# Performance work log

Measured on AMD Instinct MI355X. Metric: run time of the kernel, lower is better.

Reference implementation:

```python
import jax, jax.numpy as jnp
import numpy as np

BN_EPS = 1e-5
L2_EPS = 1e-12


def setup_inputs() -> dict:
    key = jax.random.key(0)
    ks = jax.random.split(key, 4)
    B, C, H, W = 16, 384, 56, 56
    x = jax.random.normal(ks[0], (B, C, H, W), dtype=jnp.float32)
    w_qkv = jax.random.normal(ks[1], (3 * C, C), dtype=jnp.float32) * (1.0 / np.sqrt(C))
    b_qkv = jnp.zeros((3 * C,), dtype=jnp.float32)
    w_proj = jax.random.normal(ks[2], (C, C), dtype=jnp.float32) * (1.0 / np.sqrt(C))
    b_proj = jnp.zeros((C,), dtype=jnp.float32)
    bn_gamma = jnp.ones((C,), dtype=jnp.float32)
    bn_beta = jnp.zeros((C,), dtype=jnp.float32)
    bn_mean = jnp.zeros((C,), dtype=jnp.float32)
    bn_var = jnp.ones((C,), dtype=jnp.float32)
    temperature = jnp.ones((1,), dtype=jnp.float32)
    return {"x": x, "w_qkv": w_qkv, "b_qkv": b_qkv, "w_proj": w_proj,
            "b_proj": b_proj, "bn_gamma": bn_gamma, "bn_beta": bn_beta,
            "bn_mean": bn_mean, "bn_var": bn_var, "temperature": temperature}


def _l2norm_lastdim(t):
    # F.normalize(t, dim=-1): divide by max(||t||_2, eps)
    n = jnp.sqrt(jnp.sum(t * t, axis=-1, keepdims=True))
    return t / jnp.maximum(n, L2_EPS)


def reference(x, w_qkv, b_qkv, w_proj, b_proj, bn_gamma, bn_beta, bn_mean, bn_var, temperature):
    B, C, H, W = x.shape
    N = H * W
    # BatchNorm2d (eval mode, running stats)
    scale = bn_gamma / jnp.sqrt(bn_var + BN_EPS)          # [C]
    shift = bn_beta - bn_mean * scale                     # [C]
    xn = x * scale[None, :, None, None] + shift[None, :, None, None]
    # 1x1 conv qkv: C -> 3C, operate on flattened spatial [B, C, N]
    xn_f = xn.reshape(B, C, N)
    qkv = jnp.einsum('oc,bcn->bon', w_qkv, xn_f) + b_qkv[None, :, None]  # [B,3C,N]
    q, k, v = qkv[:, :C], qkv[:, C:2 * C], qkv[:, 2 * C:]
    q = _l2norm_lastdim(q)                                # [B,C,N]
    k = _l2norm_lastdim(k)
    # channel-transposed attention: [B,C,C]
    logits = jnp.einsum('bcn,bdn->bcd', q, k) * temperature[0]
    attn = jax.nn.softmax(logits, axis=-1)
    fused = jnp.einsum('bcd,bdn->bcn', attn, v)           # [B,C,N]
    # 1x1 proj conv + residual
    out = jnp.einsum('oc,bcn->bon', w_proj, fused) + b_proj[None, :, None]
    return x + out.reshape(B, C, H, W)
```

## Files before the change

kernel.cpp:

```cpp
#include <hip/hip_runtime.h>

#define BATCH 16
#define CCH   384
#define NSP   3136
#define OQKV  1152

typedef unsigned short u16;
typedef float  f32x4  __attribute__((ext_vector_type(4)));
typedef __bf16 bf16x8 __attribute__((ext_vector_type(8)));

__device__ __forceinline__ float bf2f(u16 u) {
  union { unsigned int i; float f; } v; v.i = ((unsigned int)u) << 16; return v.f;
}
__device__ __forceinline__ u16 f2bf(float f) {
  union { float f; unsigned int i; } v; v.f = f;
  unsigned int i = v.i;
  return (u16)((i + 0x7fffu + ((i >> 16) & 1u)) >> 16);
}
__device__ __forceinline__ float rdf(const void* p, long i, bool bf) {
  return bf ? bf2f(((const u16*)p)[i]) : ((const float*)p)[i];
}

__global__ void transpose_kernel(const void* __restrict__ x, u16* __restrict__ xt,
                                 const u16* __restrict__ probe) {
  const bool bf = (probe[0] == 0x3F80u);
  __shared__ float Ls[32 * 65];
  const int t = threadIdx.x;
  const int n0 = blockIdx.x * 64, c0 = blockIdx.y * 32, b = blockIdx.z;
  {
    const int c_l = t >> 3, n8 = (t & 7) * 8;
    const long src = ((long)b * CCH + c0 + c_l) * NSP + n0 + n8;
    float v[8];
    if (bf) {
      union { uint4 q; u16 e[8]; } u; u.q = *(const uint4*)((const u16*)x + src);
      #pragma unroll
      for (int i = 0; i < 8; i++) v[i] = bf2f(u.e[i]);
    } else {
      float4 a = *(const float4*)((const float*)x + src);
      float4 c = *(const float4*)((const float*)x + src + 4);
      v[0]=a.x; v[1]=a.y; v[2]=a.z; v[3]=a.w; v[4]=c.x; v[5]=c.y; v[6]=c.z; v[7]=c.w;
    }
    #pragma unroll
    for (int i = 0; i < 8; i++) Ls[c_l * 65 + n8 + i] = v[i];
  }
  __syncthreads();
  {
    const int n_l = t >> 2, c8 = (t & 3) * 8;
    union { uint4 q; u16 e[8]; } o;
    #pragma unroll
    for (int i = 0; i < 8; i++) o.e[i] = f2bf(Ls[(c8 + i) * 65 + n_l]);
    *(uint4*)(xt + ((long)b * NSP + n0 + n_l) * CCH + c0 + c8) = o.q;
  }
}

__global__ void prep_kernel(const void* __restrict__ w_qkv, const void* __restrict__ b_qkv,
                            const void* __restrict__ gamma, const void* __restrict__ beta,
                            const void* __restrict__ mean,  const void* __restrict__ var,
                            const void* __restrict__ b_proj, const void* __restrict__ w_proj,
                            u16* __restrict__ w_eff, float* __restrict__ b_eff,
                            float* __restrict__ bproj_f, u16* __restrict__ wp_bf,
                            const u16* __restrict__ probe) {
  const bool bf = (probe[0] == 0x3F80u);
  __shared__ float s_scale[CCH], s_shift[CCH];
  const int tid = threadIdx.x;
  for (int c = tid; c < CCH; c += 128) {
    float g = rdf(gamma, c, bf), bt = rdf(beta, c, bf);
    float mn = rdf(mean, c, bf), vr = rdf(var, c, bf);
    float sc = g * rsqrtf(vr + 1e-5f);
    s_scale[c] = sc; s_shift[c] = bt - mn * sc;
  }
  __syncthreads();
  const int o = blockIdx.x;
  float part = 0.f;
  for (int c = tid; c < CCH; c += 128) {
    float w = rdf(w_qkv, (long)o * CCH + c, bf);
    w_eff[o * CCH + c] = f2bf(w * s_scale[c]);
    part += w * s_shift[c];
  }
  for (int off = 32; off > 0; off >>= 1) part += __shfl_down(part, off, 64);
  __shared__ float s_part[2];
  if ((tid & 63) == 0) s_part[tid >> 6] = part;
  __syncthreads();
  if (tid == 0) b_eff[o] = rdf(b_qkv, o, bf) + s_part[0] + s_part[1];
  if (o < CCH) {
    for (int c = tid; c < CCH; c += 128)
      wp_bf[o * CCH + c] = f2bf(rdf(w_proj, (long)o * CCH + c, bf));
  }
  if (o == 0) {
    for (int c = tid; c < CCH; c += 128) bproj_f[c] = rdf(b_proj, c, bf);
  }
}

template<int BM, int BN, int WGM, int WGN, int OUTM, bool BIASM, bool BIASN, bool RES>
__launch_bounds__(256)
__global__ void gemm_nt(const u16* __restrict__ A, const u16* __restrict__ B,
                        void* __restrict__ Cv,
                        const float* __restrict__ biasm, const float* __restrict__ biasn,
                        const void* __restrict__ resv,
                        int K, int lda, int ldb, int ldc,
                        long sA, long sB, long sC, long sRes, int zb,
                        const u16* __restrict__ probe) {
  constexpr int WM = BM / WGM, WN = BN / WGN;
  constexpr int FM = WM / 16,  FN = WN / 16;
  constexpr int NA = BM / 32,  NB = BN / 32;
  const bool f32io = (probe[0] != 0x3F80u);
  __shared__ u16 As[BM * 64];
  __shared__ u16 Bs[BN * 64];
  const int tid = threadIdx.x, wave = tid >> 6, lane = tid & 63;
  const int quad = lane >> 4, l16 = lane & 15;
  const int wm = wave / WGN, wn = wave % WGN;
  const int z = blockIdx.z;
  A += z * sA; B += z * sB;
  const long cOff = (long)(zb + z) * sC;
  const long rOff = (long)(zb + z) * sRes;
  const int m0 = blockIdx.x * BM, n0 = blockIdx.y * BN;

  f32x4 acc[FM][FN] = {};

  for (int k0 = 0; k0 < K; k0 += 64) {
    uint4 av[NA], bv[NB];
    #pragma unroll
    for (int p = 0; p < NA; p++) {
      int u = tid + p * 256;
      av[p] = *(const uint4*)(A + (long)(m0 + (u >> 3)) * lda + k0 + (u & 7) * 8);
    }
    #pragma unroll
    for (int p = 0; p < NB; p++) {
      int u = tid + p * 256;
      bv[p] = *(const uint4*)(B + (long)(n0 + (u >> 3)) * ldb + k0 + (u & 7) * 8);
    }
    #pragma unroll
    for (int p = 0; p < NA; p++) {
      int u = tid + p * 256, r = u >> 3;
      *(uint4*)&As[r * 64 + (((u & 7) ^ (r & 7)) << 3)] = av[p];
    }
    #pragma unroll
    for (int p = 0; p < NB; p++) {
      int u = tid + p * 256, r = u >> 3;
      *(uint4*)&Bs[r * 64 + (((u & 7) ^ (r & 7)) << 3)] = bv[p];
    }
    __syncthreads();

    #pragma unroll
    for (int t = 0; t < 2; t++) {
      bf16x8 af[FM], bfr[FN];
      #pragma unroll
      for (int f = 0; f < FM; f++) {
        int r = wm * WM + f * 16 + l16;
        af[f] = *(const bf16x8*)&As[r * 64 + (((t * 4 + quad) ^ (l16 & 7)) << 3)];
      }
      #pragma unroll
      for (int g = 0; g < FN; g++) {
        int r = wn * WN + g * 16 + l16;
        bfr[g] = *(const bf16x8*)&Bs[r * 64 + (((t * 4 + quad) ^ (l16 & 7)) << 3)];
      }
      #pragma unroll
      for (int f = 0; f < FM; f++)
        #pragma unroll
        for (int g = 0; g < FN; g++)
          acc[f][g] = __builtin_amdgcn_mfma_f32_16x16x32_bf16(af[f], bfr[g], acc[f][g], 0, 0, 0);
    }
    __syncthreads();
  }

  #pragma unroll
  for (int f = 0; f < FM; f++) {
    #pragma unroll
    for (int g = 0; g < FN; g++) {
      #pragma unroll
      for (int reg = 0; reg < 4; reg++) {
        int mm = m0 + wm * WM + f * 16 + quad * 4 + reg;
        int nn = n0 + wn * WN + g * 16 + l16;
        float v = acc[f][g][reg];
        if (BIASM) v += biasm[mm];
        if (BIASN) v += biasn[nn];
        long off = (long)mm * ldc + nn;
        if (RES) {
          long ro = rOff + off;
          v += f32io ? ((const float*)resv)[ro] : bf2f(((const u16*)resv)[ro]);
        }
        if (OUTM == 1)      ((float*)Cv)[cOff + off] = v;
        else if (OUTM == 2) { if (f32io) ((float*)Cv)[cOff + off] = v;
                              else       ((u16*)Cv)[cOff + off]   = f2bf(v); }
        else                ((u16*)Cv)[cOff + off] = f2bf(v);
      }
    }
  }
}

__global__ void norms_kernel(const u16* __restrict__ qk, float* __restrict__ invn) {
  const int row = blockIdx.x, b = blockIdx.y;
  const u16* p = qk + (long)b * 768 * NSP + (long)row * NSP;
  float s = 0.f;
  for (int i = threadIdx.x * 8; i < NSP; i += 256 * 8) {
    union { uint4 v; u16 u[8]; } x; x.v = *(const uint4*)(p + i);
    #pragma unroll
    for (int j = 0; j < 8; j++) { float t = bf2f(x.u[j]); s += t * t; }
  }
  for (int off = 32; off > 0; off >>= 1) s += __shfl_down(s, off, 64);
  __shared__ float sp[4];
  if ((threadIdx.x & 63) == 0) sp[threadIdx.x >> 6] = s;
  __syncthreads();
  if (threadIdx.x == 0) {
    float t = sp[0] + sp[1] + sp[2] + sp[3];
    invn[b * 768 + row] = 1.f / fmaxf(sqrtf(t), 1e-12f);
  }
}

__global__ void softmax_kernel(const float* __restrict__ logits, const float* __restrict__ invn,
                               const void* __restrict__ temp, u16* __restrict__ attn,
                               const u16* __restrict__ probe) {
  const bool bfm = (probe[0] == 0x3F80u);
  const int c = blockIdx.x, b = blockIdx.y;
  const float* row = logits + ((long)b * CCH + c) * CCH;
  const float rq = invn[b * 768 + c];
  const float T = rdf(temp, 0, bfm);
  const int tid = threadIdx.x;
  float v[3]; float mx = -1e30f;
  #pragma unroll
  for (int j = 0; j < 3; j++) {
    int d = tid + j * 128;
    float xv = row[d] * rq * invn[b * 768 + 384 + d] * T;
    v[j] = xv; mx = fmaxf(mx, xv);
  }
  for (int off = 32; off > 0; off >>= 1) mx = fmaxf(mx, __shfl_down(mx, off, 64));
  __shared__ float sm[2];
  if ((tid & 63) == 0) sm[tid >> 6] = mx;
  __syncthreads();
  mx = fmaxf(sm[0], sm[1]);
  float s = 0.f;
  #pragma unroll
  for (int j = 0; j < 3; j++) { v[j] = __expf(v[j] - mx); s += v[j]; }
  for (int off = 32; off > 0; off >>= 1) s += __shfl_down(s, off, 64);
  __shared__ float ss[2];
  if ((tid & 63) == 0) ss[tid >> 6] = s;
  __syncthreads();
  s = ss[0] + ss[1];
  const float inv = 1.f / s;
  u16* arow = attn + ((long)b * CCH + c) * CCH;
  #pragma unroll
  for (int j = 0; j < 3; j++) arow[tid + j * 128] = f2bf(v[j] * inv);
}

extern "C" void kernel_launch(void* const* d_in, const int* in_sizes, int n_in,
                              void* d_out, int out_size, void* d_ws, size_t ws_size,
                              hipStream_t stream) {
  const void* x      = d_in[0];
  const void* w_qkv  = d_in[1];
  const void* b_qkv  = d_in[2];
  const void* w_proj = d_in[3];
  const void* b_proj = d_in[4];
  const void* gamma  = d_in[5];
  const void* beta   = d_in[6];
  const void* mean   = d_in[7];
  const void* var    = d_in[8];
  const void* temp   = d_in[9];
  const u16* probe = (const u16*)gamma;

  const size_t SZ_XT    = (size_t)BATCH * NSP * CCH * 2;
  const size_t SZ_WEFF  = (size_t)OQKV * CCH * 2;
  const size_t SZ_WPBF  = (size_t)CCH * CCH * 2;
  const size_t SZ_BEFF  = (size_t)OQKV * 4;
  const size_t SZ_BPROJ = (size_t)CCH * 4;
  const size_t SZ_INVN  = (size_t)BATCH * 768 * 4;
  const size_t SZ_QK_B  = (size_t)768 * NSP * 2;
  const size_t SZ_VT_B  = (size_t)NSP * CCH * 2;
  const size_t SZ_FT_B  = (size_t)NSP * CCH * 2;
  const size_t SZ_LOG_B = (size_t)CCH * CCH * 4;
  const size_t SZ_ATT_B = (size_t)CCH * CCH * 2;
  const size_t P = SZ_QK_B + SZ_VT_B + SZ_FT_B + SZ_LOG_B + SZ_ATT_B;
  const size_t FIXED = SZ_XT + SZ_WEFF + SZ_WPBF + SZ_BEFF + SZ_BPROJ + SZ_INVN;

  long chunk = 1;
  if (ws_size >= FIXED + P) {
    chunk = (long)((ws_size - FIXED) / P);
    if (chunk > BATCH) chunk = BATCH;
    if (chunk < 1) chunk = 1;
  }

  char* ws = (char*)d_ws;
  u16*   xt      = (u16*)ws;   ws += SZ_XT;
  u16*   w_eff   = (u16*)ws;   ws += SZ_WEFF;
  u16*   wp_bf   = (u16*)ws;   ws += SZ_WPBF;
  float* b_eff   = (float*)ws; ws += SZ_BEFF;
  float* bproj_f = (float*)ws; ws += SZ_BPROJ;
  float* invn    = (float*)ws; ws += SZ_INVN;
  float* logits  = (float*)ws; ws += SZ_LOG_B * chunk;
  u16*   attn    = (u16*)ws;   ws += SZ_ATT_B * chunk;
  u16*   qk      = (u16*)ws;   ws += SZ_QK_B * chunk;
  u16*   v_t     = (u16*)ws;   ws += SZ_VT_B * chunk;
  u16*   fused_t = (u16*)ws;   ws += SZ_FT_B * chunk;

  transpose_kernel<<<dim3(NSP / 64, CCH / 32, BATCH), dim3(256), 0, stream>>>(x, xt, probe);
  prep_kernel<<<dim3(OQKV), dim3(128), 0, stream>>>(
      w_qkv, b_qkv, gamma, beta, mean, var, b_proj, w_proj,
      w_eff, b_eff, bproj_f, wp_bf, probe);

  const long sX  = (long)CCH * NSP;
  const long sXT = (long)NSP * CCH;
  const long sQK = (long)768 * NSP;
  const long sVT = (long)NSP * CCH;
  const long sFT = (long)NSP * CCH;
  const long sLG = (long)CCH * CCH;
  const long sAT = (long)CCH * CCH;

  for (long b0 = 0; b0 < BATCH; b0 += chunk) {
    const int nb = (int)((BATCH - b0) < chunk ? (BATCH - b0) : chunk);
    const u16* xtb = xt + b0 * sXT;

    gemm_nt<256, 64, 4, 1, 0, true, false, false>
        <<<dim3(3, 49, nb), dim3(256), 0, stream>>>(
        w_eff, xtb, qk, b_eff, nullptr, nullptr,
        CCH, CCH, CCH, NSP, 0L, sXT, sQK, 0L, 0, probe);

    gemm_nt<64, 384, 1, 4, 0, false, true, false>
        <<<dim3(49, 1, nb), dim3(256), 0, stream>>>(
        xtb, w_eff + (long)768 * CCH, v_t, nullptr, b_eff + 768, nullptr,
        CCH, CCH, CCH, CCH, sXT, 0L, sVT, 0L, 0, probe);

    norms_kernel<<<dim3(768, nb), dim3(256), 0, stream>>>(qk, invn + b0 * 768);

    gemm_nt<96, 96, 2, 2, 1, false, false, false>
        <<<dim3(4, 4, nb), dim3(256), 0, stream>>>(
        qk, qk + (long)CCH * NSP, logits, nullptr, nullptr, nullptr,
        NSP, NSP, NSP, CCH, sQK, sQK, sLG, 0L, 0, probe);

    softmax_kernel<<<dim3(CCH, nb), dim3(128), 0, stream>>>(
        logits, invn + b0 * 768, temp, attn, probe);

    gemm_nt<64, 384, 1, 4, 0, false, false, false>
        <<<dim3(49, 1, nb), dim3(256), 0, stream>>>(
        v_t, attn, fused_t, nullptr, nullptr, nullptr,
        CCH, CCH, CCH, CCH, sVT, sAT, sFT, 0L, 0, probe);

    gemm_nt<384, 64, 4, 1, 2, true, false, true>
        <<<dim3(1, 49, nb), dim3(256), 0, stream>>>(
        wp_bf, fused_t, d_out, bproj_f, nullptr, x,
        CCH, CCH, CCH, NSP, 0L, sFT, sX, sX, (int)b0, probe);
  }
}
```

Baseline: 456.8 us.

## Use direct global-to-LDS loads, split-K logits GEMM, and smaller GEMM tiles

The GEMM tile loads now use global_load_lds, which writes global memory straight into shared memory and skips the register staging. The XOR swizzle moves onto the global source address so the LDS layout stays the same. The long-K logits GEMM is split 7 ways with atomicAdd into a pre-zeroed fp32 buffer, giving the small 4x4 grid more blocks. Several 384-wide tiles are halved to 192 to raise block count and lower LDS use. In exchange the change adds an extra zeroing kernel and atomic contention, and the async LDS load is still followed by a plain __syncthreads with no explicit wait on the load counter.

```diff
diff --git a/kernel.cpp b/kernel.cpp
--- a/kernel.cpp
+++ b/kernel.cpp
@@ -19,6 +19,12 @@
 }
 __device__ __forceinline__ float rdf(const void* p, long i, bool bf) {
   return bf ? bf2f(((const u16*)p)[i]) : ((const float*)p)[i];
+}
+
+__device__ __forceinline__ void gload_lds16(const u16* g, u16* l) {
+  __builtin_amdgcn_global_load_lds(
+      (const __attribute__((address_space(1))) void*)g,
+      (__attribute__((address_space(3))) void*)l, 16, 0, 0);
 }
 
 __global__ void transpose_kernel(const void* __restrict__ x, u16* __restrict__ xt,
@@ -91,7 +97,13 @@
   }
 }
 
-template<int BM, int BN, int WGM, int WGN, int OUTM, bool BIASM, bool BIASN, bool RES>
+__global__ void zero_kernel(float4* __restrict__ p, long n4) {
+  for (long i = (long)blockIdx.x * blockDim.x + threadIdx.x; i < n4;
+       i += (long)gridDim.x * blockDim.x)
+    p[i] = make_float4(0.f, 0.f, 0.f, 0.f);
+}
+
+template<int BM, int BN, int WGM, int WGN, int OUTM, bool BIASM, bool BIASN, bool RES, int KS>
 __launch_bounds__(256)
 __global__ void gemm_nt(const u16* __restrict__ A, const u16* __restrict__ B,
                         void* __restrict__ Cv,
@@ -104,41 +116,41 @@
   constexpr int FM = WM / 16,  FN = WN / 16;
   constexpr int NA = BM / 32,  NB = BN / 32;
   const bool f32io = (probe[0] != 0x3F80u);
-  __shared__ u16 As[BM * 64];
-  __shared__ u16 Bs[BN * 64];
+  __shared__ __align__(16) u16 As[BM * 64];
+  __shared__ __align__(16) u16 Bs[BN * 64];
   const int tid = threadIdx.x, wave = tid >> 6, lane = tid & 63;
   const int quad = lane >> 4, l16 = lane & 15;
   const int wm = wave / WGN, wn = wave % WGN;
-  const int z = blockIdx.z;
+  int z = blockIdx.z, kc = 0;
+  if (KS > 1) { kc = z % KS; z /= KS; }
   A += z * sA; B += z * sB;
   const long cOff = (long)(zb + z) * sC;
   const long rOff = (long)(zb + z) * sRes;
   const int m0 = blockIdx.x * BM, n0 = blockIdx.y * BN;
+  const int kLen = K / KS, kBeg = kc * kLen;
+
+  const u16* ag[NA]; u16* al[NA];
+  const u16* bg[NB]; u16* bl[NB];
+  #pragma unroll
+  for (int p = 0; p < NA; p++) {
+    int u = tid + p * 256, r = u >> 3, k8 = u & 7;
+    ag[p] = A + (long)(m0 + r) * lda + kBeg + ((k8 ^ (r & 7)) << 3);
+    al[p] = &As[(wave * 64 + p * 256) * 8];
+  }
+  #pragma unroll
+  for (int p = 0; p < NB; p++) {
+    int u = tid + p * 256, r = u >> 3, k8 = u & 7;
+    bg[p] = B + (long)(n0 + r) * ldb + kBeg + ((k8 ^ (r & 7)) << 3);
+    bl[p] = &Bs[(wave * 64 + p * 256) * 8];
+  }
 
   f32x4 acc[FM][FN] = {};
 
-  for (int k0 = 0; k0 < K; k0 += 64) {
-    uint4 av[NA], bv[NB];
-    #pragma unroll
-    for (int p = 0; p < NA; p++) {
-      int u = tid + p * 256;
-      av[p] = *(const uint4*)(A + (long)(m0 + (u >> 3)) * lda + k0 + (u & 7) * 8);
-    }
-    #pragma unroll
-    for (int p = 0; p < NB; p++) {
-      int u = tid + p * 256;
-      bv[p] = *(const uint4*)(B + (long)(n0 + (u >> 3)) * ldb + k0 + (u & 7) * 8);
-    }
-    #pragma unroll
-    for (int p = 0; p < NA; p++) {
-      int u = tid + p * 256, r = u >> 3;
-      *(uint4*)&As[r * 64 + (((u & 7) ^ (r & 7)) << 3)] = av[p];
-    }
-    #pragma unroll
-    for (int p = 0; p < NB; p++) {
-      int u = tid + p * 256, r = u >> 3;
-      *(uint4*)&Bs[r * 64 + (((u & 7) ^ (r & 7)) << 3)] = bv[p];
-    }
+  for (int ks = 0; ks < kLen; ks += 64) {
+    #pragma unroll
+    for (int p = 0; p < NA; p++) { gload_lds16(ag[p], al[p]); ag[p] += 64; }
+    #pragma unroll
+    for (int p = 0; p < NB; p++) { gload_lds16(bg[p], bl[p]); bg[p] += 64; }
     __syncthreads();
 
     #pragma unroll
@@ -182,6 +194,7 @@
         if (OUTM == 1)      ((float*)Cv)[cOff + off] = v;
         else if (OUTM == 2) { if (f32io) ((float*)Cv)[cOff + off] = v;
                               else       ((u16*)Cv)[cOff + off]   = f2bf(v); }
+        else if (OUTM == 3) atomicAdd((float*)Cv + cOff + off, v);
         else                ((u16*)Cv)[cOff + off] = f2bf(v);
       }
     }
@@ -308,33 +321,36 @@
     const int nb = (int)((BATCH - b0) < chunk ? (BATCH - b0) : chunk);
     const u16* xtb = xt + b0 * sXT;
 
-    gemm_nt<256, 64, 4, 1, 0, true, false, false>
+    gemm_nt<256, 64, 4, 1, 0, true, false, false, 1>
         <<<dim3(3, 49, nb), dim3(256), 0, stream>>>(
         w_eff, xtb, qk, b_eff, nullptr, nullptr,
         CCH, CCH, CCH, NSP, 0L, sXT, sQK, 0L, 0, probe);
 
-    gemm_nt<64, 384, 1, 4, 0, false, true, false>
-        <<<dim3(49, 1, nb), dim3(256), 0, stream>>>(
+    gemm_nt<64, 192, 2, 2, 0, false, true, false, 1>
+        <<<dim3(49, 2, nb), dim3(256), 0, stream>>>(
         xtb, w_eff + (long)768 * CCH, v_t, nullptr, b_eff + 768, nullptr,
         CCH, CCH, CCH, CCH, sXT, 0L, sVT, 0L, 0, probe);
 
     norms_kernel<<<dim3(768, nb), dim3(256), 0, stream>>>(qk, invn + b0 * 768);
 
-    gemm_nt<96, 96, 2, 2, 1, false, false, false>
-        <<<dim3(4, 4, nb), dim3(256), 0, stream>>>(
+    zero_kernel<<<dim3(512), dim3(256), 0, stream>>>(
+        (float4*)logits, (long)nb * sLG / 4);
+
+    gemm_nt<96, 96, 2, 2, 3, false, false, false, 7>
+        <<<dim3(4, 4, nb * 7), dim3(256), 0, stream>>>(
         qk, qk + (long)CCH * NSP, logits, nullptr, nullptr, nullptr,
         NSP, NSP, NSP, CCH, sQK, sQK, sLG, 0L, 0, probe);
 
     softmax_kernel<<<dim3(CCH, nb), dim3(128), 0, stream>>>(
         logits, invn + b0 * 768, temp, attn, probe);
 
-    gemm_nt<64, 384, 1, 4, 0, false, false, false>
-        <<<dim3(49, 1, nb), dim3(256), 0, stream>>>(
+    gemm_nt<64, 192, 2, 2, 0, false, false, false, 1>
+        <<<dim3(49, 2, nb), dim3(256), 0, stream>>>(
         v_t, attn, fused_t, nullptr, nullptr, nullptr,
         CCH, CCH, CCH, CCH, sVT, sAT, sFT, 0L, 0, probe);
 
-    gemm_nt<384, 64, 4, 1, 2, true, false, true>
-        <<<dim3(1, 49, nb), dim3(256), 0, stream>>>(
+    gemm_nt<192, 64, 2, 2, 2, true, false, true, 1>
+        <<<dim3(2, 49, nb), dim3(256), 0, stream>>>(
         wp_bf, fused_t, d_out, bproj_f, nullptr, x,
         CCH, CCH, CCH, NSP, 0L, sFT, sX, sX, (int)b0, probe);
   }
```

Result: no change. 461.0 us (+0.9%).
